# Optimization experiments

Hardware: AMD Instinct MI355X
Metric: run time of the kernel (lower is better)

## Reference

```python
import jax, jax.numpy as jnp
import numpy as np

B, S, F, D, H, L, K = 64, 512, 8, 512, 8, 2, 512
FF = 4 * D
DH = D // H


def _ln(x):
    m = jnp.mean(x, axis=-1, keepdims=True)
    v = jnp.var(x, axis=-1, keepdims=True)
    return (x - m) * jax.lax.rsqrt(v + 1e-5)


def _encoder_layer(x, Wqkv, Wo, W1, b1, W2, b2):
    # pre-LN multi-head self-attention
    h = _ln(x)
    qkv = h @ Wqkv                                   # [B,S,3D]
    q, k, v = jnp.split(qkv, 3, axis=-1)
    q = q.reshape(B, S, H, DH)
    k = k.reshape(B, S, H, DH)
    v = v.reshape(B, S, H, DH)
    scores = jnp.einsum('bqhd,bkhd->bhqk', q, k) / jnp.sqrt(jnp.float32(DH))
    attn = jax.nn.softmax(scores, axis=-1)
    o = jnp.einsum('bhqk,bkhd->bqhd', attn, v).reshape(B, S, D) @ Wo
    x = x + o
    # pre-LN feed-forward
    h = _ln(x)
    x = x + (jax.nn.relu(h @ W1 + b1) @ W2 + b2)
    return x


def setup_inputs() -> dict:
    key = jax.random.key(0)
    ks = jax.random.split(key, 12)
    sc = 0.02
    inp = {
        'x': jax.random.normal(ks[0], (B, S, F), dtype=jnp.float32),
        'enc_W': jax.random.normal(ks[1], (F, D), dtype=jnp.float32) * sc,
        'enc_b': jnp.zeros((D,), dtype=jnp.float32),
        'Wqkv': jax.random.normal(ks[2], (L, D, 3 * D), dtype=jnp.float32) * sc,
        'Wo': jax.random.normal(ks[3], (L, D, D), dtype=jnp.float32) * sc,
        'W1': jax.random.normal(ks[4], (L, D, FF), dtype=jnp.float32) * sc,
        'b1': jnp.zeros((L, FF), dtype=jnp.float32),
        'W2': jax.random.normal(ks[5], (L, FF, D), dtype=jnp.float32) * sc,
        'b2': jnp.zeros((L, D), dtype=jnp.float32),
        'centers': jax.random.normal(ks[6], (K, D), dtype=jnp.float32),
    }
    return inp


def reference(x, enc_W, enc_b, Wqkv, Wo, W1, b1, W2, b2, centers):
    # enc_embedding
    h = x @ enc_W + enc_b                            # [B,S,D]
    # seq_model: stack of standard transformer encoder layers
    for i in range(L):
        h = _encoder_layer(h, Wqkv[i], Wo[i], W1[i], b1[i], W2[i], b2[i])
    output_seq = h                                   # [B,S,D]
    # torch.cdist(output_seq, centers, p=2) via matmul expansion
    on2 = jnp.sum(output_seq * output_seq, axis=-1, keepdims=True)   # [B,S,1]
    cn2 = jnp.sum(centers * centers, axis=-1)                        # [K]
    dist2 = on2 + cn2[None, None, :] - 2.0 * jnp.einsum('bsd,kd->bsk', output_seq, centers)
    cluster_ids = jnp.argmin(dist2, axis=-1)                         # [B,S]
    assigned_centroids = centers[cluster_ids]                        # [B,S,D] gather
    diff = output_seq - assigned_centroids
    # torch.norm(diff, dim=1)**2 then mean == mean over (B,D) of sum over S of diff^2
    loss = jnp.mean(jnp.sum(diff * diff, axis=1))
    return loss, output_seq
```

## Files before the change

kernel.cpp:

```cpp
#include <hip/hip_runtime.h>
#include <cstdint>
#include <cstddef>

typedef __attribute__((ext_vector_type(4))) float f32x4;
typedef __attribute__((ext_vector_type(8))) short s16x8;
typedef __attribute__((ext_vector_type(4))) short s16x4;

__device__ __forceinline__ short f2bf(float f){
  unsigned u; __builtin_memcpy(&u, &f, 4);
  u += 0x7fffu + ((u >> 16) & 1u);
  return (short)(u >> 16);
}

__device__ __forceinline__ void gll16(const void* g, void* l) {
  auto* lp = (__attribute__((address_space(3))) unsigned*)(uintptr_t)(l);
  const auto* gp = (const __attribute__((address_space(1))) unsigned*)(uintptr_t)(g);
  __builtin_amdgcn_global_load_lds(gp, lp, 16, 0, 0);
}

__device__ __forceinline__ void ds_tr8(unsigned a, s16x4* r) {
  asm volatile(
    "ds_read_b64_tr_b16 %0, %8\n\t"
    "ds_read_b64_tr_b16 %1, %8 offset:512\n\t"
    "ds_read_b64_tr_b16 %2, %8 offset:2048\n\t"
    "ds_read_b64_tr_b16 %3, %8 offset:2560\n\t"
    "ds_read_b64_tr_b16 %4, %8 offset:4096\n\t"
    "ds_read_b64_tr_b16 %5, %8 offset:4608\n\t"
    "ds_read_b64_tr_b16 %6, %8 offset:6144\n\t"
    "ds_read_b64_tr_b16 %7, %8 offset:6656\n\t"
    "s_waitcnt lgkmcnt(0)"
    : "=&v"(r[0]), "=&v"(r[1]), "=&v"(r[2]), "=&v"(r[3]),
      "=&v"(r[4]), "=&v"(r[5]), "=&v"(r[6]), "=&v"(r[7])
    : "v"(a)
    : "memory");
}

__global__ __launch_bounds__(256) void encode_kernel(
    const float* __restrict__ x, const float* __restrict__ W,
    const float* __restrict__ b, float* __restrict__ out)
{
  const int t = blockIdx.x;
  float xv[8];
#pragma unroll
  for (int f = 0; f < 8; ++f) xv[f] = x[(size_t)t*8 + f];
  for (int d = threadIdx.x; d < 512; d += 256) {
    float acc = b[d];
#pragma unroll
    for (int f = 0; f < 8; ++f) acc += xv[f] * W[f*512 + d];
    out[(size_t)t*512 + d] = acc;
  }
}

__global__ __launch_bounds__(256) void ln_kernel(
    const float* __restrict__ x, short* __restrict__ out)
{
  const int w = threadIdx.x >> 6, lane = threadIdx.x & 63;
  const int t = blockIdx.x * 4 + w;
  const float* row = x + (size_t)t * 512;
  float4 v0 = *(const float4*)&row[lane*8];
  float4 v1 = *(const float4*)&row[lane*8 + 4];
  float vals[8] = {v0.x,v0.y,v0.z,v0.w,v1.x,v1.y,v1.z,v1.w};
  float s = 0.f, sq = 0.f;
#pragma unroll
  for (int i = 0; i < 8; ++i) { s += vals[i]; sq += vals[i]*vals[i]; }
#pragma unroll
  for (int m = 1; m < 64; m <<= 1) { s += __shfl_xor(s, m); sq += __shfl_xor(sq, m); }
  float mean = s * (1.f/512.f);
  float var  = sq * (1.f/512.f) - mean*mean;
  float rstd = rsqrtf(var + 1e-5f);
  s16x8 o;
#pragma unroll
  for (int i = 0; i < 8; ++i) o[i] = f2bf((vals[i]-mean)*rstd);
  *(s16x8*)&out[(size_t)t*512 + lane*8] = o;
}

__global__ __launch_bounds__(256) void transpose_bf16_kernel(
    const float* __restrict__ in, short* __restrict__ out, int K, int N, int kshift)
{
  const int o = blockIdx.x * 256 + threadIdx.x;
  const int k = o & (K - 1), n = o >> kshift;
  out[o] = f2bf(in[(size_t)k * N + n]);
}

__global__ __launch_bounds__(256) void convert_bf16_kernel(
    const float* __restrict__ in, short* __restrict__ out)
{
  const int i = blockIdx.x * 256 + threadIdx.x;
  out[i] = f2bf(in[i]);
}

template<bool BIAS, bool RELU, bool RESID, bool OUT32>
__global__ __launch_bounds__(512, 1) void gemm_kernel(
    const short* __restrict__ A, const short* __restrict__ Bt,
    void* Cout, const float* __restrict__ bias,
    const float* resid, int M, int N, int K)
{
  __shared__ short As[4][256 * 32];
  __shared__ short Bs[4][256 * 32];
  const int tid = threadIdx.x;
  const int lane = tid & 63, w = tid >> 6;
  const int wr = w >> 2, wc = w & 3;
  const int q = lane & 15, g = lane >> 4;

  const int nx = gridDim.x;
  const int d = blockIdx.y * nx + blockIdx.x;
  const int per = (nx * gridDim.y) >> 3;
  const int lid = (d & 7) * per + (d >> 3);
  const int bx = lid % nx, by = lid / nx;
  const int m0 = by * 256, n0 = bx * 256;

  const int srow = lane >> 2;
  const int scol = (((lane & 3) ^ ((lane >> 4) & 3)) * 8);
  const short* aS0 = A  + (size_t)(m0 + w*32 + srow) * K + scol;
  const short* aS1 = aS0 + (size_t)16 * K;
  const short* bS0 = Bt + (size_t)(n0 + w*32 + srow) * K + scol;
  const short* bS1 = bS0 + (size_t)16 * K;
  const int d0 = (w*2) * 512, d1 = (w*2 + 1) * 512;

  const int gs = (g ^ (q >> 2)) * 8;

  f32x4 acc[8][4] = {};
  const int nt = K >> 5;

  auto STAGE = [&](int tt) {
    const int k0 = tt << 5;
    const int nb = tt & 3;
    gll16(aS0 + k0, &As[nb][d0]);
    gll16(aS1 + k0, &As[nb][d1]);
    gll16(bS0 + k0, &Bs[nb][d0]);
    gll16(bS1 + k0, &Bs[nb][d1]);
  };
  auto COMPUTE = [&](int t) {
    const int bufc = t & 3;
    const short* Ab = &As[bufc][0];
    const short* Bb = &Bs[bufc][0];
    if (t + 3 < nt) STAGE(t + 3);
    s16x8 bF[4];
#pragma unroll
    for (int i = 0; i < 4; ++i) bF[i] = *(const s16x8*)&Bb[(wc*64 + i*16 + q)*32 + gs];
#pragma unroll
    for (int ph = 0; ph < 4; ++ph) {
      s16x8 a0 = *(const s16x8*)&Ab[(wr*128 + (2*ph    )*16 + q)*32 + gs];
      s16x8 a1 = *(const s16x8*)&Ab[(wr*128 + (2*ph + 1)*16 + q)*32 + gs];
      __builtin_amdgcn_s_setprio(1);
#pragma unroll
      for (int ni = 0; ni < 4; ++ni)
        acc[2*ph][ni] = __builtin_amdgcn_mfma_f32_16x16x32_bf16(a0, bF[ni], acc[2*ph][ni], 0, 0, 0);
#pragma unroll
      for (int ni = 0; ni < 4; ++ni)
        acc[2*ph+1][ni] = __builtin_amdgcn_mfma_f32_16x16x32_bf16(a1, bF[ni], acc[2*ph+1][ni], 0, 0, 0);
      __builtin_amdgcn_s_setprio(0);
      __builtin_amdgcn_sched_barrier(0);
    }
  };

  STAGE(0); STAGE(1); STAGE(2);

  for (int t = 0; t < nt - 2; ++t) {
    asm volatile("s_waitcnt vmcnt(8)" ::: "memory");
    __builtin_amdgcn_s_barrier();
    __builtin_amdgcn_sched_barrier(0);
    COMPUTE(t);
  }
  asm volatile("s_waitcnt vmcnt(4)" ::: "memory");
  __builtin_amdgcn_s_barrier();
  __builtin_amdgcn_sched_barrier(0);
  COMPUTE(nt - 2);
  asm volatile("s_waitcnt vmcnt(0)" ::: "memory");
  __builtin_amdgcn_s_barrier();
  __builtin_amdgcn_sched_barrier(0);
  COMPUTE(nt - 1);

#pragma unroll
  for (int mi = 0; mi < 8; ++mi) {
#pragma unroll
    for (int r = 0; r < 4; ++r) {
      const int gr = m0 + wr*128 + mi*16 + g*4 + r;
#pragma unroll
      for (int ni = 0; ni < 4; ++ni) {
        const int gc = n0 + wc*64 + ni*16 + q;
        float v = acc[mi][ni][r];
        if (BIAS) v += bias[gc];
        if (RELU) v = fmaxf(v, 0.f);
        if (RESID) v += resid[(size_t)gr * N + gc];
        if (OUT32) ((float*)Cout)[(size_t)gr * N + gc] = v;
        else       ((short*)Cout)[(size_t)gr * N + gc] = f2bf(v);
      }
    }
  }
}

__global__ __launch_bounds__(256) void attn_kernel(
    const short* __restrict__ qkv, short* __restrict__ attn_out)
{
  __shared__ short Ks[2][64 * 64];
  __shared__ short Vs[2][64 * 64];
  const int tid = threadIdx.x;
  const int w = tid >> 6, lane = tid & 63;
  const int q16 = lane & 15, g = lane >> 4;
  const int dd = blockIdx.x;
  const int lid = (dd & 7) * (int)(gridDim.x >> 3) + (dd >> 3);
  const int qt4 = lid & 7, h = (lid >> 3) & 7, b = lid >> 6;
  const size_t base = (size_t)b * 512 * 1536;
  const int qrow = qt4*64 + w*16 + q16;

  s16x8 bQ0, bQ1;
  {
    const size_t p = base + (size_t)qrow * 1536 + h*64 + g*8;
    bQ0 = *(const s16x8*)&qkv[p];
    bQ1 = *(const s16x8*)&qkv[p + 32];
  }

  const int c0 = w*2, c1 = w*2 + 1;
  const short* kS0 = qkv + base + (size_t)(c0*8 + (lane>>3))*1536 + 512 + h*64 + ((lane&7)^(lane>>3))*8;
  const short* kS1 = qkv + base + (size_t)(c1*8 + (lane>>3))*1536 + 512 + h*64 + ((lane&7)^(lane>>3))*8;
  const short* vS0 = qkv + base + (size_t)((c0&1)*32 + (lane>>1))*1536 + 1024 + h*64 + (c0>>1)*16 + (lane&1)*8;
  const short* vS1 = qkv + base + (size_t)((c1&1)*32 + (lane>>1))*1536 + 1024 + h*64 + (c1>>1)*16 + (lane&1)*8;

  const unsigned vs_lane = (unsigned)(size_t)(&Vs[0][0]) + (unsigned)((q16 + g*64)*2);
  const int sw = q16 & 7;

  float mrun = -1e30f, ssum = 0.f;
  f32x4 O[4] = {};

  gll16(kS0, &Ks[0][c0*512]);
  gll16(kS1, &Ks[0][c1*512]);
  gll16(vS0, &Vs[0][c0*512]);
  gll16(vS1, &Vs[0][c1*512]);
  __syncthreads();

  int cur = 0;
  for (int j0 = 0; j0 < 512; j0 += 64) {
    s16x8 ka0[4], ka1[4];
#pragma unroll
    for (int grp = 0; grp < 4; ++grp) {
      const int rb = (grp*16 + q16) * 64;
      ka0[grp] = *(const s16x8*)&Ks[cur][rb + ((g    ) ^ sw)*8];
      ka1[grp] = *(const s16x8*)&Ks[cur][rb + ((g + 4) ^ sw)*8];
    }
    if (j0 + 64 < 512) {
      const size_t joff = (size_t)(j0 + 64) * 1536;
      const int nxt = cur ^ 1;
      gll16(kS0 + joff, &Ks[nxt][c0*512]);
      gll16(kS1 + joff, &Ks[nxt][c1*512]);
      gll16(vS0 + joff, &Vs[nxt][c0*512]);
      gll16(vS1 + joff, &Vs[nxt][c1*512]);
    }
    __builtin_amdgcn_sched_barrier(0);

    f32x4 c[4];
    __builtin_amdgcn_s_setprio(1);
#pragma unroll
    for (int grp = 0; grp < 4; ++grp) {
      f32x4 z = {};
      c[grp] = __builtin_amdgcn_mfma_f32_16x16x32_bf16(ka0[grp], bQ0, z, 0, 0, 0);
      c[grp] = __builtin_amdgcn_mfma_f32_16x16x32_bf16(ka1[grp], bQ1, c[grp], 0, 0, 0);
    }
    __builtin_amdgcn_s_setprio(0);

    float sc[16];
#pragma unroll
    for (int grp = 0; grp < 4; ++grp)
#pragma unroll
      for (int r = 0; r < 4; ++r) sc[grp*4 + r] = c[grp][r] * 0.125f;
    float bm = sc[0];
#pragma unroll
    for (int i = 1; i < 16; ++i) bm = fmaxf(bm, sc[i]);
    bm = fmaxf(bm, __shfl_xor(bm, 16));
    bm = fmaxf(bm, __shfl_xor(bm, 32));
    const float mn = fmaxf(mrun, bm);
    const float alpha = __expf(mrun - mn);
    float p[16]; float bs = 0.f;
#pragma unroll
    for (int i = 0; i < 16; ++i) { p[i] = __expf(sc[i] - mn); bs += p[i]; }
    bs += __shfl_xor(bs, 16);
    bs += __shfl_xor(bs, 32);
    ssum = ssum * alpha + bs;
    mrun = mn;
#pragma unroll
    for (int db = 0; db < 4; ++db) O[db] *= alpha;

#pragma unroll
    for (int kk = 0; kk < 2; ++kk) {
      s16x8 pf;
#pragma unroll
      for (int e = 0; e < 8; ++e) pf[e] = f2bf(p[(kk*2 + (e >> 2))*4 + (e & 3)]);
      s16x4 r[8];
      ds_tr8(vs_lane + (unsigned)(cur << 13) + (unsigned)(kk*1024), r);
      __builtin_amdgcn_sched_barrier(0);
      __builtin_amdgcn_s_setprio(1);
#pragma unroll
      for (int db = 0; db < 4; ++db) {
        s16x8 vf = __builtin_shufflevector(r[2*db], r[2*db + 1], 0, 1, 2, 3, 4, 5, 6, 7);
        O[db] = __builtin_amdgcn_mfma_f32_16x16x32_bf16(vf, pf, O[db], 0, 0, 0);
      }
      __builtin_amdgcn_s_setprio(0);
    }
    __syncthreads();
    cur ^= 1;
  }

  const float inv = 1.f / ssum;
  const size_t tok = (size_t)b*512 + qrow;
#pragma unroll
  for (int db = 0; db < 4; ++db) {
    s16x4 ov;
#pragma unroll
    for (int r = 0; r < 4; ++r) ov[r] = f2bf(O[db][r] * inv);
    *(s16x4*)&attn_out[tok*512 + h*64 + db*16 + g*4] = ov;
  }
}

__global__ __launch_bounds__(256) void finalize_seq_kernel(
    const float* __restrict__ resid, float* __restrict__ outseq, short* __restrict__ obf)
{
  const size_t i = (size_t)blockIdx.x * 256 + threadIdx.x;
  const float v = resid[i];
  outseq[i] = v;
  obf[i] = f2bf(v);
}

__global__ __launch_bounds__(256) void cn2_kernel(
    const float* __restrict__ centers, float* __restrict__ cn2)
{
  const int c = blockIdx.x;
  __shared__ float red[256];
  float s = 0.f;
  for (int d = threadIdx.x; d < 512; d += 256) { float v = centers[(size_t)c*512 + d]; s += v*v; }
  red[threadIdx.x] = s; __syncthreads();
  for (int off = 128; off > 0; off >>= 1) {
    if (threadIdx.x < off) red[threadIdx.x] += red[threadIdx.x + off];
    __syncthreads();
  }
  if (threadIdx.x == 0) cn2[c] = red[0];
}

__global__ __launch_bounds__(256) void argmin_kernel(
    const float* __restrict__ gdist, const float* __restrict__ cn2,
    const float* __restrict__ resid, const float* __restrict__ centers,
    float* __restrict__ partial)
{
  const int w = threadIdx.x >> 6, lane = threadIdx.x & 63;
  const int t = blockIdx.x * 4 + w;
  float best = 1e30f; int bi = 0;
#pragma unroll
  for (int j = 0; j < 8; ++j) {
    const int k = j*64 + lane;
    const float v = cn2[k] - 2.f * gdist[(size_t)t*512 + k];
    if (v < best || (v == best && k < bi)) { best = v; bi = k; }
  }
#pragma unroll
  for (int mm = 1; mm < 64; mm <<= 1) {
    const float ov = __shfl_xor(best, mm); const int oi = __shfl_xor(bi, mm);
    if (ov < best || (ov == best && oi < bi)) { best = ov; bi = oi; }
  }
  float s = 0.f;
#pragma unroll
  for (int j = 0; j < 2; ++j) {
    float4 o = *(const float4*)&resid[(size_t)t*512 + lane*8 + j*4];
    float4 c = *(const float4*)&centers[(size_t)bi*512 + lane*8 + j*4];
    const float dx = o.x-c.x, dy = o.y-c.y, dz = o.z-c.z, dw = o.w-c.w;
    s += dx*dx + dy*dy + dz*dz + dw*dw;
  }
#pragma unroll
  for (int mm = 1; mm < 64; mm <<= 1) s += __shfl_xor(s, mm);
  __shared__ float red[4];
  if (lane == 0) red[w] = s;
  __syncthreads();
  if (threadIdx.x == 0) partial[blockIdx.x] = red[0] + red[1] + red[2] + red[3];
}

__global__ __launch_bounds__(256) void loss_kernel(
    const float* __restrict__ partial, int n, float* __restrict__ out)
{
  float s = 0.f;
  for (int i = threadIdx.x; i < n; i += 256) s += partial[i];
  __shared__ float red[256];
  red[threadIdx.x] = s; __syncthreads();
  for (int off = 128; off > 0; off >>= 1) {
    if (threadIdx.x < off) red[threadIdx.x] += red[threadIdx.x + off];
    __syncthreads();
  }
  if (threadIdx.x == 0) out[0] = red[0] * (1.f / 32768.f);
}

extern "C" void kernel_launch(void* const* d_in, const int* in_sizes, int n_in,
                              void* d_out, int out_size, void* d_ws, size_t ws_size,
                              hipStream_t stream) {
  const float* x     = (const float*)d_in[0];
  const float* enc_W = (const float*)d_in[1];
  const float* enc_b = (const float*)d_in[2];
  const float* Wqkv  = (const float*)d_in[3];
  const float* Wo    = (const float*)d_in[4];
  const float* W1    = (const float*)d_in[5];
  const float* b1    = (const float*)d_in[6];
  const float* W2    = (const float*)d_in[7];
  const float* b2    = (const float*)d_in[8];
  const float* cen   = (const float*)d_in[9];
  float* out = (float*)d_out;

  const int NT = 32768;
  char* ws = (char*)d_ws;
  float* resid   = (float*)(ws);
  short* h_ln    = (short*)(ws + 67108864);
  char*  pool    = ws + 100663296;
  short* qkv     = (short*)pool;
  short* attn_o  = (short*)(pool + 100663296);
  short* hidden  = (short*)pool;
  float* gdist   = (float*)pool;
  short* wbase   = (short*)(ws + 234881024);
  short* wqT     = wbase;
  short* woT     = wbase + 1572864;
  short* w1T     = wbase + 2097152;
  short* w2T     = wbase + 4194304;
  short* cenb    = wbase + 6291456;
  float* cn2     = (float*)(ws + 247988224);
  float* partial = (float*)(ws + 247990272);

  for (int l = 0; l < 2; ++l) {
    transpose_bf16_kernel<<<3072, 256, 0, stream>>>(Wqkv + (size_t)l*512*1536, wqT + (size_t)l*786432, 512, 1536, 9);
    transpose_bf16_kernel<<<1024, 256, 0, stream>>>(Wo   + (size_t)l*512*512,  woT + (size_t)l*262144, 512, 512, 9);
    transpose_bf16_kernel<<<4096, 256, 0, stream>>>(W1   + (size_t)l*512*2048, w1T + (size_t)l*1048576, 512, 2048, 9);
    transpose_bf16_kernel<<<4096, 256, 0, stream>>>(W2   + (size_t)l*2048*512, w2T + (size_t)l*1048576, 2048, 512, 11);
  }
  convert_bf16_kernel<<<1024, 256, 0, stream>>>(cen, cenb);
  cn2_kernel<<<512, 256, 0, stream>>>(cen, cn2);

  encode_kernel<<<NT, 256, 0, stream>>>(x, enc_W, enc_b, resid);

  for (int l = 0; l < 2; ++l) {
    ln_kernel<<<NT/4, 256, 0, stream>>>(resid, h_ln);
    gemm_kernel<false,false,false,false><<<dim3(6, 128), 512, 0, stream>>>(
        h_ln, wqT + (size_t)l*786432, qkv, nullptr, nullptr, NT, 1536, 512);
    attn_kernel<<<4096, 256, 0, stream>>>(qkv, attn_o);
    gemm_kernel<false,false,true,true><<<dim3(2, 128), 512, 0, stream>>>(
        attn_o, woT + (size_t)l*262144, resid, nullptr, resid, NT, 512, 512);
    ln_kernel<<<NT/4, 256, 0, stream>>>(resid, h_ln);
    gemm_kernel<true,true,false,false><<<dim3(8, 128), 512, 0, stream>>>(
        h_ln, w1T + (size_t)l*1048576, hidden, b1 + (size_t)l*2048, nullptr, NT, 2048, 512);
    gemm_kernel<true,false,true,true><<<dim3(2, 128), 512, 0, stream>>>(
        hidden, w2T + (size_t)l*1048576, resid, b2 + (size_t)l*512, resid, NT, 512, 2048);
  }

  finalize_seq_kernel<<<65536, 256, 0, stream>>>(resid, out + 1, h_ln);
  gemm_kernel<false,false,false,true><<<dim3(2, 128), 512, 0, stream>>>(
      h_ln, cenb, gdist, nullptr, nullptr, NT, 512, 512);
  argmin_kernel<<<NT/4, 256, 0, stream>>>(gdist, cn2, resid, cen, partial);
  loss_kernel<<<1, 256, 0, stream>>>(partial, NT/4, out);
}
```

Measured before the change: 953.0 us.

## Split GEMM K-tile into two half-phases with interleaved A/B prefetch

```diff
diff --git a/kernel.cpp b/kernel.cpp
--- a/kernel.cpp
+++ b/kernel.cpp
@@ -122,54 +122,61 @@
   f32x4 acc[8][4] = {};
   const int nt = K >> 5;
 
-  auto STAGE = [&](int tt) {
-    const int k0 = tt << 5;
-    const int nb = tt & 3;
+  auto STAGE_A = [&](int tt) {
+    const int k0 = tt << 5, nb = tt & 3;
     gll16(aS0 + k0, &As[nb][d0]);
     gll16(aS1 + k0, &As[nb][d1]);
+  };
+  auto STAGE_B = [&](int tt) {
+    const int k0 = tt << 5, nb = tt & 3;
     gll16(bS0 + k0, &Bs[nb][d0]);
     gll16(bS1 + k0, &Bs[nb][d1]);
   };
-  auto COMPUTE = [&](int t) {
+
+  auto TILE = [&](int t, bool pre) {
     const int bufc = t & 3;
     const short* Ab = &As[bufc][0];
     const short* Bb = &Bs[bufc][0];
-    if (t + 3 < nt) STAGE(t + 3);
-    s16x8 bF[4];
+    s16x8 bF[4], aF[4];
 #pragma unroll
     for (int i = 0; i < 4; ++i) bF[i] = *(const s16x8*)&Bb[(wc*64 + i*16 + q)*32 + gs];
 #pragma unroll
-    for (int ph = 0; ph < 4; ++ph) {
-      s16x8 a0 = *(const s16x8*)&Ab[(wr*128 + (2*ph    )*16 + q)*32 + gs];
-      s16x8 a1 = *(const s16x8*)&Ab[(wr*128 + (2*ph + 1)*16 + q)*32 + gs];
-      __builtin_amdgcn_s_setprio(1);
+    for (int i = 0; i < 4; ++i) aF[i] = *(const s16x8*)&Ab[(wr*128 + i*16 + q)*32 + gs];
+    if (pre) STAGE_A(t + 2);
+    __builtin_amdgcn_sched_barrier(0);
+    __builtin_amdgcn_s_setprio(1);
+#pragma unroll
+    for (int mi = 0; mi < 4; ++mi)
 #pragma unroll
       for (int ni = 0; ni < 4; ++ni)
-        acc[2*ph][ni] = __builtin_amdgcn_mfma_f32_16x16x32_bf16(a0, bF[ni], acc[2*ph][ni], 0, 0, 0);
+        acc[mi][ni] = __builtin_amdgcn_mfma_f32_16x16x32_bf16(aF[mi], bF[ni], acc[mi][ni], 0, 0, 0);
+    __builtin_amdgcn_s_setprio(0);
+    __builtin_amdgcn_s_barrier();
+    s16x8 aG[4];
+#pragma unroll
+    for (int i = 0; i < 4; ++i) aG[i] = *(const s16x8*)&Ab[(wr*128 + (4+i)*16 + q)*32 + gs];
+    if (pre) STAGE_B(t + 2);
+    __builtin_amdgcn_sched_barrier(0);
+    __builtin_amdgcn_s_setprio(1);
+#pragma unroll
+    for (int mi = 0; mi < 4; ++mi)
 #pragma unroll
       for (int ni = 0; ni < 4; ++ni)
-        acc[2*ph+1][ni] = __builtin_amdgcn_mfma_f32_16x16x32_bf16(a1, bF[ni], acc[2*ph+1][ni], 0, 0, 0);
-      __builtin_amdgcn_s_setprio(0);
-      __builtin_amdgcn_sched_barrier(0);
-    }
+        acc[4+mi][ni] = __builtin_amdgcn_mfma_f32_16x16x32_bf16(aG[mi], bF[ni], acc[4+mi][ni], 0, 0, 0);
+    __builtin_amdgcn_s_setprio(0);
+    __builtin_amdgcn_s_barrier();
   };
 
-  STAGE(0); STAGE(1); STAGE(2);
-
-  for (int t = 0; t < nt - 2; ++t) {
-    asm volatile("s_waitcnt vmcnt(8)" ::: "memory");
+  STAGE_A(0); STAGE_B(0); STAGE_A(1); STAGE_B(1);
+
+  for (int t = 0; t < nt - 1; ++t) {
+    asm volatile("s_waitcnt vmcnt(4)" ::: "memory");
     __builtin_amdgcn_s_barrier();
-    __builtin_amdgcn_sched_barrier(0);
-    COMPUTE(t);
-  }
-  asm volatile("s_waitcnt vmcnt(4)" ::: "memory");
-  __builtin_amdgcn_s_barrier();
-  __builtin_amdgcn_sched_barrier(0);
-  COMPUTE(nt - 2);
+    TILE(t, t + 2 < nt);
+  }
   asm volatile("s_waitcnt vmcnt(0)" ::: "memory");
   __builtin_amdgcn_s_barrier();
-  __builtin_amdgcn_sched_barrier(0);
-  COMPUTE(nt - 1);
+  TILE(nt - 1, false);
 
 #pragma unroll
   for (int mi = 0; mi < 8; ++mi) {
```

Result: no change. 947.8 us (-0.5%).
